# Optimization experiments

Measured on AMD Instinct MI355X. Metric: run time of the kernel, lower is better.

## Reference

```python
import jax, jax.numpy as jnp
import numpy as np

MASK_VAL = -1e30


def setup_inputs() -> dict:
    key = jax.random.key(0)
    ks = jax.random.split(key, 9)
    B, C, Q, D = 64, 2048, 128, 128
    s = 0.05  # small param init scale (xavier-like)
    return {
        "vfeats": jax.random.normal(ks[0], (B, C, D), jnp.float32),
        "qfeats": jax.random.normal(ks[1], (B, Q, D), jnp.float32),
        "vmask": jnp.ones((B, C), jnp.float32),
        "qmask": jnp.ones((B, Q), jnp.float32),
        "w4C": jax.random.normal(ks[2], (D, 1), jnp.float32) * s,
        "w4Q": jax.random.normal(ks[3], (D, 1), jnp.float32) * s,
        "w4mlu": jax.random.normal(ks[4], (1, 1, D), jnp.float32) * s,
        "cqa_W": jax.random.normal(ks[5], (D, 4 * D), jnp.float32) * s,  # Conv1D k=1 == Linear(4D->D)
        "cqa_b": jnp.zeros((D,), jnp.float32),
        "wp": jax.random.normal(ks[6], (D, 1), jnp.float32) * s,
        "cc_W": jax.random.normal(ks[7], (D, 2 * D), jnp.float32) * s,  # Conv1D k=1 == Linear(2D->D)
        "cc_b": jnp.zeros((D,), jnp.float32),
    }


def reference(vfeats, qfeats, vmask, qmask, w4C, w4Q, w4mlu, cqa_W, cqa_b, wp, cc_W, cc_b):
    # --- CQAttention ---
    # trilinear score: [B, C, Q]  (dropout is identity at inference)
    score = (vfeats @ w4C) \
        + jnp.swapaxes(qfeats @ w4Q, 1, 2) \
        + jnp.einsum('bcd,bqd->bcq', vfeats * w4mlu, qfeats)
    score_ = jax.nn.softmax(score + (1.0 - qmask[:, None, :]) * MASK_VAL, axis=2)   # [B,C,Q]
    score_t = jax.nn.softmax(score + (1.0 - vmask[:, :, None]) * MASK_VAL, axis=1)  # [B,C,Q]
    c2q = score_ @ qfeats                                                           # [B,C,D]
    # q2c = (score_ @ score_t^T) @ context; reassociate to avoid the [B,C,C] matrix
    q2c = score_ @ jnp.einsum('bcq,bcd->bqd', score_t, vfeats)                      # [B,C,D]
    cat = jnp.concatenate([vfeats, c2q, vfeats * c2q, vfeats * q2c], axis=2)        # [B,C,4D]
    feats = cat @ cqa_W.T + cqa_b                                                   # [B,C,D]
    # --- CQConcatenate (weighted pool of query) ---
    alpha = jax.nn.softmax((qfeats @ wp) + (1.0 - qmask[:, :, None]) * MASK_VAL, axis=1)  # [B,Q,1]
    pooled = jnp.einsum('bqd,bq->bd', qfeats, alpha[..., 0])                        # [B,D]
    pooled = jnp.broadcast_to(pooled[:, None, :], feats.shape)                      # [B,C,D]
    out = jnp.concatenate([feats, pooled], axis=2) @ cc_W.T + cc_b                  # [B,C,D]
    return jax.nn.relu(out)
```

## Files before the change

### kernel.cpp

```cpp
#include <hip/hip_runtime.h>
#include <stdint.h>

#define DI __device__ __forceinline__

typedef __attribute__((ext_vector_type(8))) short short8;
typedef __attribute__((ext_vector_type(4))) short short4v;
typedef __attribute__((ext_vector_type(4))) float float4v;
typedef __attribute__((ext_vector_type(2))) float float2v;
typedef __attribute__((ext_vector_type(4))) unsigned int uint4v;
typedef __attribute__((ext_vector_type(2))) unsigned int uint2v;
typedef __attribute__((ext_vector_type(2))) __bf16 bf162;

#define MFMA16(a, b, c) __builtin_amdgcn_mfma_f32_16x16x32_bf16((a), (b), (c), 0, 0, 0)

DI float b2f(short s) {
    uint32_t u = ((uint32_t)(uint16_t)s) << 16;
    float f;
    __builtin_memcpy(&f, &u, 4);
    return f;
}
DI unsigned int cvtpk(float a, float b) {
    bf162 h = __builtin_convertvector((float2v){a, b}, bf162);
    return __builtin_bit_cast(unsigned int, h);
}
DI float u2f(unsigned int u) { return __builtin_bit_cast(float, u); }


__global__ __launch_bounds__(256) void k_packfuse(const float* __restrict__ vf, const float* __restrict__ qf,
                                                  const float* __restrict__ w4C, const float* __restrict__ w4Q,
                                                  const float* __restrict__ w4mlu, const float* __restrict__ vmask,
                                                  const float* __restrict__ qmask, short* __restrict__ vfA,
                                                  short* __restrict__ vfT, short* __restrict__ qfBW,
                                                  short* __restrict__ qTf, float* __restrict__ cvp,
                                                  float* __restrict__ qvp, const float* __restrict__ cqaW,
                                                  short* __restrict__ cqaWp, const float* __restrict__ ccW,
                                                  short* __restrict__ ccWp, const float* __restrict__ wp,
                                                  const float* __restrict__ ccb, float* __restrict__ pc) {
    __shared__ float St[32 * 133];
    __shared__ float Rd[128], Af[128], Pp[2][128], Pl[128];
    int bx = blockIdx.x, by = blockIdx.y;
    int t = threadIdx.x;
    if (bx == 69) {
        if (by < 32) {
            int idx = by * 256 + t;
            int lane = idx & 63, ks = (idx >> 6) & 3, part = (idx >> 8) & 3, nt = idx >> 10;
            const float* p = cqaW + (size_t)(nt * 16 + (lane & 15)) * 512 + part * 128 + ks * 32 + (lane >> 4) * 8;
            float4v a = *(const float4v*)p, b = *(const float4v*)(p + 4);
            uint4v ou;
            ou[0] = cvtpk(a[0], a[1]);
            ou[1] = cvtpk(a[2], a[3]);
            ou[2] = cvtpk(b[0], b[1]);
            ou[3] = cvtpk(b[2], b[3]);
            *(short8*)(cqaWp + (size_t)idx * 8) = __builtin_bit_cast(short8, ou);
        } else if (by < 40) {
            int idx = (by - 32) * 256 + t;
            int lane = idx & 63, ks = (idx >> 6) & 3, ot = idx >> 8;
            const float* p = ccW + (size_t)(ot * 16 + (lane & 15)) * 256 + ks * 32 + (lane >> 4) * 8;
            float4v a = *(const float4v*)p, b = *(const float4v*)(p + 4);
            uint4v ou;
            ou[0] = cvtpk(a[0], a[1]);
            ou[1] = cvtpk(a[2], a[3]);
            ou[2] = cvtpk(b[0], b[1]);
            ou[3] = cvtpk(b[2], b[3]);
            *(short8*)(ccWp + (size_t)idx * 8) = __builtin_bit_cast(short8, ou);
        }
        return;
    }
    if (bx == 68) {
        int b = by;
        int q = t >> 1, hf = t & 1;
        const float* qrow = qf + ((size_t)(b * 128 + q) << 7) + hf * 64;
        float s = 0.f;
#pragma unroll 4
        for (int d = 0; d < 64; d += 4) {
            float4v xv = *(const float4v*)(qrow + d);
            float4v wg = *(const float4v*)(wp + hf * 64 + d);
            s += xv[0] * wg[0] + xv[1] * wg[1] + xv[2] * wg[2] + xv[3] * wg[3];
        }
        s += __shfl_xor(s, 1, 64);
        s += (1.f - qmask[b * 128 + q]) * (-1e30f);
        if (hf == 0) Rd[q] = s;
        __syncthreads();
        for (int off = 64; off >= 1; off >>= 1) {
            if (t < off) Rd[t] = fmaxf(Rd[t], Rd[t + off]);
            __syncthreads();
        }
        float m = Rd[0];
        __syncthreads();
        float e = __expf(s - m);
        if (hf == 0) Rd[q] = e;
        __syncthreads();
        for (int off = 64; off >= 1; off >>= 1) {
            if (t < off) Rd[t] += Rd[t + off];
            __syncthreads();
        }
        if (hf == 0) Af[q] = e * __builtin_amdgcn_rcpf(Rd[0]);
        __syncthreads();
        {
            int d = t & 127, qh = t >> 7;
            float pacc = 0.f;
            for (int qq = qh * 64; qq < qh * 64 + 64; ++qq) pacc += qf[((size_t)(b * 128 + qq) << 7) + d] * Af[qq];
            Pp[qh][d] = pacc;
        }
        __syncthreads();
        if (t < 128) Pl[t] = Pp[0][t] + Pp[1][t];
        __syncthreads();
        {
            int o = t & 127, dh = t >> 7;
            float acc = 0.f;
            for (int d = dh * 64; d < dh * 64 + 64; ++d) acc += Pl[d] * ccW[o * 256 + 128 + d];
            Pp[dh][o] = acc;
        }
        __syncthreads();
        if (t < 128) pc[b * 128 + t] = ccb[t] + Pp[0][t] + Pp[1][t];
        return;
    }
    const float* src;
    const float* wm;
    const float* wv;
    const float* mask;
    short* dstA;
    short* dstT;
    float* dotout;
    int kc, nkc, b = by;
    if (bx < 64) {
        src = vf; wm = nullptr; wv = w4C; mask = vmask;
        dstA = vfA; dstT = vfT; dotout = cvp; kc = bx; nkc = 64;
    } else {
        src = qf; wm = w4mlu; wv = w4Q; mask = qmask;
        dstA = qfBW; dstT = qTf; dotout = qvp; kc = bx - 64; nkc = 4;
    }
    int rl = t >> 3, sub = t & 7, dseg = sub * 16;
    int grow = (b * nkc + kc) * 32 + rl;
    const float* p = src + ((size_t)grow << 7) + dseg;
    float4v v[4];
#pragma unroll
    for (int g = 0; g < 4; ++g) v[g] = *(const float4v*)(p + g * 4);
    float s = 0.f;
#pragma unroll
    for (int g = 0; g < 4; ++g) {
        float4v wg = *(const float4v*)(wv + dseg + g * 4);
#pragma unroll
        for (int j = 0; j < 4; ++j) s += v[g][j] * wg[j];
    }
#pragma unroll
    for (int off = 1; off < 8; off <<= 1) s += __shfl_xor(s, off, 64);
    if (sub == 0) dotout[grow] = s + (1.f - mask[grow]) * (-1e30f);
#pragma unroll
    for (int g = 0; g < 4; ++g)
#pragma unroll
        for (int j = 0; j < 4; ++j) St[rl * 133 + dseg + g * 4 + j] = v[g][j];
#pragma unroll
    for (int h = 0; h < 2; ++h) {
        int c16 = sub * 2 + h;
        int ks = c16 >> 2, quad = c16 & 3;
        float4v m0 = wm ? *(const float4v*)(wm + c16 * 8) : (float4v){1.f, 1.f, 1.f, 1.f};
        float4v m1 = wm ? *(const float4v*)(wm + c16 * 8 + 4) : (float4v){1.f, 1.f, 1.f, 1.f};
        uint4v ou;
        ou[0] = cvtpk(v[h * 2][0] * m0[0], v[h * 2][1] * m0[1]);
        ou[1] = cvtpk(v[h * 2][2] * m0[2], v[h * 2][3] * m0[3]);
        ou[2] = cvtpk(v[h * 2 + 1][0] * m1[0], v[h * 2 + 1][1] * m1[1]);
        ou[3] = cvtpk(v[h * 2 + 1][2] * m1[2], v[h * 2 + 1][3] * m1[3]);
        int tile = b * (nkc * 2) + kc * 2 + (rl >> 4);
        *(short8*)(dstA + ((size_t)(tile * 4 + ks) << 9) + (quad * 16 + (rl & 15)) * 8) =
            __builtin_bit_cast(short8, ou);
    }
    __syncthreads();
#pragma unroll
    for (int i = 0; i < 2; ++i) {
        int dt = (t >> 6) + i * 4;
        int lane = t & 63, ln = lane & 15, quad = lane >> 4;
        int d = dt * 16 + ln;
        uint4v ou;
#pragma unroll
        for (int wd = 0; wd < 4; ++wd)
            ou[wd] = cvtpk(St[(quad * 8 + 2 * wd) * 133 + d], St[(quad * 8 + 2 * wd + 1) * 133 + d]);
        *(short8*)(dstT + (((size_t)(b * 8 + dt) * nkc + kc) << 9) + lane * 8) = __builtin_bit_cast(short8, ou);
    }
}

__global__ __launch_bounds__(256) void k_Tacc(const short* __restrict__ vfA, const short* __restrict__ vfT,
                                              const short* __restrict__ qfBW, const float* __restrict__ cvp,
                                              float* __restrict__ Pg, float* __restrict__ Csg) {
    __shared__ short Al[16 * 136];
    __shared__ float Red[4][16][130];
    __shared__ float csred[4][16];
    int tid = threadIdx.x, w = tid >> 6, lane = tid & 63, ln = lane & 15, quad = lane >> 4;
    int id = blockIdx.x;
    int xcd = id & 7, k = id >> 3;
    int g = xcd * 16 + (k & 15);
    int qt = k >> 4;
    int b = g & 63, s = g >> 6;
    short8 bq[4];
#pragma unroll
    for (int ks = 0; ks < 4; ++ks) bq[ks] = *(const short8*)(qfBW + (((size_t)(b * 8 + qt) * 4 + ks) << 9) + lane * 8);
    float4v acc[8];
#pragma unroll
    for (int dt = 0; dt < 8; ++dt) acc[dt] = (float4v){0.f, 0.f, 0.f, 0.f};
    float colacc = 0.f;
    for (int it = 0; it < 8; ++it) {
        int cbase = s * 1024 + it * 128 + w * 32;
        int ct = b * 128 + (cbase >> 4);
        short8 bb[8];
#pragma unroll
        for (int dt = 0; dt < 8; ++dt)
            bb[dt] = *(const short8*)(vfT + (((size_t)(b * 8 + dt) * 64 + s * 32 + it * 4 + w) << 9) + lane * 8);
        __builtin_amdgcn_sched_barrier(0);
        float4v ds[2];
        ds[0] = (float4v){0.f, 0.f, 0.f, 0.f};
        ds[1] = (float4v){0.f, 0.f, 0.f, 0.f};
#pragma unroll
        for (int ks = 0; ks < 4; ++ks) {
#pragma unroll
            for (int mt = 0; mt < 2; ++mt) {
                short8 a = *(const short8*)(vfA + (((size_t)(ct + mt) * 4 + ks) << 9) + lane * 8);
                ds[mt] = MFMA16(a, bq[ks], ds[mt]);
            }
        }
#pragma unroll
        for (int mt = 0; mt < 2; ++mt) {
            float4v cv = *(const float4v*)(cvp + b * 2048 + cbase + mt * 16 + quad * 4);
            float e0 = __expf(ds[mt][0] + cv[0]);
            float e1 = __expf(ds[mt][1] + cv[1]);
            float e2 = __expf(ds[mt][2] + cv[2]);
            float e3 = __expf(ds[mt][3] + cv[3]);
            colacc += e0 + e1 + e2 + e3;
            uint2v eu;
            eu[0] = cvtpk(e0, e1);
            eu[1] = cvtpk(e2, e3);
            *(short4v*)(Al + ln * 136 + w * 32 + mt * 16 + quad * 4) = __builtin_bit_cast(short4v, eu);
        }
        short8 a = *(const short8*)(Al + ln * 136 + w * 32 + quad * 8);
#pragma unroll
        for (int dt = 0; dt < 8; ++dt) acc[dt] = MFMA16(a, bb[dt], acc[dt]);
    }
#pragma unroll
    for (int dt = 0; dt < 8; ++dt)
#pragma unroll
        for (int r = 0; r < 4; ++r) Red[w][quad * 4 + r][dt * 16 + ln] = acc[dt][r];
    float p = colacc;
    p += __shfl_xor(p, 16, 64);
    p += __shfl_xor(p, 32, 64);
    if (lane < 16) csred[w][lane] = p;
    __syncthreads();
    if (tid < 16)
        Csg[((size_t)(s * 64 + b)) * 128 + qt * 16 + tid] =
            csred[0][tid] + csred[1][tid] + csred[2][tid] + csred[3][tid];
    {
        int q = tid >> 4, db = (tid & 15) * 8;
        float4v s0, s1;
#pragma unroll
        for (int j = 0; j < 4; ++j) {
            s0[j] = Red[0][q][db + j] + Red[1][q][db + j] + Red[2][q][db + j] + Red[3][q][db + j];
            s1[j] = Red[0][q][db + 4 + j] + Red[1][q][db + 4 + j] + Red[2][q][db + 4 + j] + Red[3][q][db + 4 + j];
        }
        size_t pb = (((size_t)(s * 64 + b)) * 8 + qt) * 2048 + q * 128 + db;
        *(float4v*)(Pg + pb) = s0;
        *(float4v*)(Pg + pb + 4) = s1;
    }
}

__global__ __launch_bounds__(256) void k_Tcomb(const float* __restrict__ Pg, const float* __restrict__ Csg,
                                               short* __restrict__ Ttf) {
    int idx = blockIdx.x * 256 + threadIdx.x;
    int lane = idx & 63, dt = (idx >> 8) & 7, b = idx >> 11;
    int d = dt * 16 + (lane & 15), q0 = ((idx >> 6) & 3) * 32 + (lane >> 4) * 8;
    float pv[8];
#pragma unroll
    for (int j = 0; j < 8; ++j) {
        int q = q0 + j;
        size_t o0 = ((size_t)(b * 8) + (q >> 4)) * 2048 + (q & 15) * 128 + d;
        size_t o1 = ((size_t)((64 + b) * 8) + (q >> 4)) * 2048 + (q & 15) * 128 + d;
        float cs = Csg[b * 128 + q] + Csg[(64 + b) * 128 + q];
        pv[j] = (Pg[o0] + Pg[o1]) * __builtin_amdgcn_rcpf(cs);
    }
    uint4v ou;
#pragma unroll
    for (int wd = 0; wd < 4; ++wd) ou[wd] = cvtpk(pv[2 * wd], pv[2 * wd + 1]);
    *(short8*)(Ttf + (size_t)idx * 8) = __builtin_bit_cast(short8, ou);
}

__global__ __launch_bounds__(256, 4) void k_out(const short* __restrict__ vfA, const short* __restrict__ qfBW,
                                                const short* __restrict__ qTf, const short* __restrict__ Ttf,
                                                const float* __restrict__ qvp, const short* __restrict__ cqaWp,
                                                const float* __restrict__ cqab, const short* __restrict__ ccWp,
                                                const float* __restrict__ pc, float* __restrict__ out) {
    __shared__ __align__(16) short Sl[64 * 128];
    __shared__ __align__(16) short Xl[64 * 128];
    int tid = threadIdx.x, w = tid >> 6, lane = tid & 63, ln = lane & 15, quad = lane >> 4;
    int jl = ln & 7, hi8 = ln >> 3;
    const float4v z4 = {0.f, 0.f, 0.f, 0.f};
    int id = blockIdx.x;
    int xcd = id & 7, k = id >> 3;
    int b = xcd * 8 + (k & 7);
    int cx = k >> 3;
    int c0 = cx * 64 + w * 16;
    int tt = b * 128 + (c0 >> 4);
    int wbase = w * 2048;
    {
        float4v sc[8];
#pragma unroll
        for (int qt = 0; qt < 8; ++qt) sc[qt] = z4;
#pragma unroll
        for (int ks = 0; ks < 4; ++ks) {
            short8 bqf[8];
#pragma unroll
            for (int qt = 0; qt < 8; ++qt)
                bqf[qt] = *(const short8*)(qfBW + (((size_t)(b * 8 + qt) * 4 + ks) << 9) + lane * 8);
            short8 av = *(const short8*)(vfA + (((size_t)tt * 4 + ks) << 9) + lane * 8);
#pragma unroll
            for (int qt = 0; qt < 8; ++qt) sc[qt] = MFMA16(av, bqf[qt], sc[qt]);
        }
        float qvl[8];
#pragma unroll
        for (int qt = 0; qt < 8; ++qt) qvl[qt] = qvp[b * 128 + qt * 16 + ln];
        short8 p2[8];
#pragma unroll
        for (int dt = 0; dt < 8; ++dt)
            p2[dt] = *(const short8*)(qTf + (((size_t)(b * 8 + dt) * 4 + 0) << 9) + lane * 8);
        __builtin_amdgcn_sched_barrier(0);
#pragma unroll
        for (int r = 0; r < 4; ++r) {
            float x[8], m = -3.4e38f;
#pragma unroll
            for (int qt = 0; qt < 8; ++qt) {
                x[qt] = sc[qt][r] + qvl[qt];
                m = fmaxf(m, x[qt]);
            }
#pragma unroll
            for (int off = 1; off < 16; off <<= 1) m = fmaxf(m, __shfl_xor(m, off, 64));
            float e[8], sm = 0.f;
#pragma unroll
            for (int qt = 0; qt < 8; ++qt) {
                e[qt] = __expf(x[qt] - m);
                sm += e[qt];
            }
#pragma unroll
            for (int off = 1; off < 16; off <<= 1) sm += __shfl_xor(sm, off, 64);
            float inv = __builtin_amdgcn_rcpf(sm);
            int rb = (quad * 4 + r) * 8 + jl;
#pragma unroll
            for (int qp = 0; qp < 4; ++qp) {
                unsigned int u = cvtpk(e[2 * qp] * inv, e[2 * qp + 1] * inv);
                Sl[wbase + qp * 512 + hi8 * 128 + rb] = (short)u;
                Sl[wbase + qp * 512 + (2 + hi8) * 128 + rb] = (short)(u >> 16);
            }
        }
        short8 sa[4];
#pragma unroll
        for (int ks = 0; ks < 4; ++ks) sa[ks] = *(const short8*)(Sl + wbase + ks * 512 + lane * 8);
        float4v a2q[8];
#pragma unroll
        for (int dt = 0; dt < 8; ++dt) a2q[dt] = MFMA16(sa[0], p2[dt], z4);
#pragma unroll
        for (int ks = 1; ks < 4; ++ks) {
            short8 bf[8];
#pragma unroll
            for (int dt = 0; dt < 8; ++dt)
                bf[dt] = *(const short8*)(qTf + (((size_t)(b * 8 + dt) * 4 + ks) << 9) + lane * 8);
#pragma unroll
            for (int dt = 0; dt < 8; ++dt) a2q[dt] = MFMA16(sa[ks], bf[dt], a2q[dt]);
        }
        short8 p3[8];
#pragma unroll
        for (int dt = 0; dt < 8; ++dt)
            p3[dt] = *(const short8*)(Ttf + (((size_t)(b * 8 + dt) * 4 + 0) << 9) + lane * 8);
        __builtin_amdgcn_sched_barrier(0);
#pragma unroll
        for (int r = 0; r < 4; ++r) {
            int rb = (quad * 4 + r) * 8 + jl;
#pragma unroll
            for (int dp = 0; dp < 4; ++dp) {
                unsigned int u = cvtpk(a2q[2 * dp][r], a2q[2 * dp + 1][r]);
                Xl[wbase + dp * 512 + hi8 * 128 + rb] = (short)u;
                Xl[wbase + dp * 512 + (2 + hi8) * 128 + rb] = (short)(u >> 16);
            }
        }
        float4v aq2[8];
#pragma unroll
        for (int dt = 0; dt < 8; ++dt) aq2[dt] = MFMA16(sa[0], p3[dt], z4);
#pragma unroll
        for (int ks = 1; ks < 4; ++ks) {
            short8 bf[8];
#pragma unroll
            for (int dt = 0; dt < 8; ++dt)
                bf[dt] = *(const short8*)(Ttf + (((size_t)(b * 8 + dt) * 4 + ks) << 9) + lane * 8);
#pragma unroll
            for (int dt = 0; dt < 8; ++dt) aq2[dt] = MFMA16(sa[ks], bf[dt], aq2[dt]);
        }
#pragma unroll
        for (int r = 0; r < 4; ++r) {
            int rb = (quad * 4 + r) * 8 + jl;
#pragma unroll
            for (int dp = 0; dp < 4; ++dp) {
                unsigned int u = cvtpk(aq2[2 * dp][r], aq2[2 * dp + 1][r]);
                Sl[wbase + dp * 512 + hi8 * 128 + rb] = (short)u;
                Sl[wbase + dp * 512 + (2 + hi8) * 128 + rb] = (short)(u >> 16);
            }
        }
    }
    __syncthreads();
    float4v accF[4][2];
#pragma unroll
    for (int ct = 0; ct < 4; ++ct)
#pragma unroll
        for (int nt2 = 0; nt2 < 2; ++nt2) accF[ct][nt2] = z4;
#pragma unroll
    for (int ks = 0; ks < 4; ++ks) {
        short8 avk[4];
#pragma unroll
        for (int ct = 0; ct < 4; ++ct)
            avk[ct] = *(const short8*)(vfA + (((size_t)(b * 128 + cx * 4 + ct) * 4 + ks) << 9) + lane * 8);
#pragma unroll
        for (int part = 0; part < 4; ++part) {
            short8 bwp[2];
#pragma unroll
            for (int nt2 = 0; nt2 < 2; ++nt2)
                bwp[nt2] =
                    *(const short8*)(cqaWp + (((size_t)((w * 2 + nt2) * 4 + part) * 4 + ks) << 9) + lane * 8);
            short8 a[4];
#pragma unroll
            for (int ct = 0; ct < 4; ++ct) {
                int fo = ct * 2048 + ks * 512 + lane * 8;
                if (part == 0) {
                    a[ct] = avk[ct];
                } else if (part == 1) {
                    a[ct] = *(const short8*)(Xl + fo);
                } else {
                    short8 mfr = (part == 2) ? *(const short8*)(Xl + fo) : *(const short8*)(Sl + fo);
                    uint4v ua = __builtin_bit_cast(uint4v, avk[ct]);
                    uint4v um = __builtin_bit_cast(uint4v, mfr);
                    uint4v uo;
#pragma unroll
                    for (int wd = 0; wd < 4; ++wd) {
                        float a0 = u2f(ua[wd] << 16), a1 = u2f(ua[wd] & 0xffff0000u);
                        float m0 = u2f(um[wd] << 16), m1 = u2f(um[wd] & 0xffff0000u);
                        uo[wd] = cvtpk(a0 * m0, a1 * m1);
                    }
                    a[ct] = __builtin_bit_cast(short8, uo);
                }
            }
#pragma unroll
            for (int nt2 = 0; nt2 < 2; ++nt2)
#pragma unroll
                for (int ct = 0; ct < 4; ++ct) accF[ct][nt2] = MFMA16(a[ct], bwp[nt2], accF[ct][nt2]);
        }
    }
    __syncthreads();
    {
        float b0 = cqab[(w * 2) * 16 + ln], b1 = cqab[(w * 2 + 1) * 16 + ln];
#pragma unroll
        for (int ct = 0; ct < 4; ++ct)
#pragma unroll
            for (int r = 0; r < 4; ++r) {
                unsigned int u = cvtpk(accF[ct][0][r] + b0, accF[ct][1][r] + b1);
                int rb = ct * 2048 + w * 512 + (quad * 4 + r) * 8 + jl;
                Sl[rb + hi8 * 128] = (short)u;
                Sl[rb + (2 + hi8) * 128] = (short)(u >> 16);
            }
    }
    __syncthreads();
    float4v accO[4][2];
#pragma unroll
    for (int ct = 0; ct < 4; ++ct)
#pragma unroll
        for (int ot2 = 0; ot2 < 2; ++ot2) accO[ct][ot2] = z4;
#pragma unroll
    for (int ks = 0; ks < 4; ++ks) {
        short8 bwo[2];
#pragma unroll
        for (int ot2 = 0; ot2 < 2; ++ot2)
            bwo[ot2] = *(const short8*)(ccWp + (((size_t)((w * 2 + ot2) * 4 + ks)) << 9) + lane * 8);
        short8 a[4];
#pragma unroll
        for (int ct = 0; ct < 4; ++ct) a[ct] = *(const short8*)(Sl + ct * 2048 + ks * 512 + lane * 8);
#pragma unroll
        for (int ot2 = 0; ot2 < 2; ++ot2)
#pragma unroll
            for (int ct = 0; ct < 4; ++ct) accO[ct][ot2] = MFMA16(a[ct], bwo[ot2], accO[ct][ot2]);
    }
#pragma unroll
    for (int ct = 0; ct < 4; ++ct)
#pragma unroll
        for (int ot2 = 0; ot2 < 2; ++ot2) {
            int o = (w * 2 + ot2) * 16 + ln;
            float pco = pc[b * 128 + o];
#pragma unroll
            for (int r = 0; r < 4; ++r) {
                int c = cx * 64 + ct * 16 + quad * 4 + r;
                out[((size_t)(b * 2048 + c) << 7) + o] = fmaxf(accO[ct][ot2][r] + pco, 0.f);
            }
        }
}

extern "C" void kernel_launch(void* const* d_in, const int* in_sizes, int n_in, void* d_out, int out_size, void* d_ws,
                              size_t ws_size, hipStream_t stream) {
    const float* vf = (const float*)d_in[0];
    const float* qf = (const float*)d_in[1];
    const float* vmask = (const float*)d_in[2];
    const float* qmask = (const float*)d_in[3];
    const float* w4C = (const float*)d_in[4];
    const float* w4Q = (const float*)d_in[5];
    const float* w4mlu = (const float*)d_in[6];
    const float* cqaW = (const float*)d_in[7];
    const float* cqab = (const float*)d_in[8];
    const float* wp = (const float*)d_in[9];
    const float* ccW = (const float*)d_in[10];
    const float* ccb = (const float*)d_in[11];
    float* out = (float*)d_out;
    char* ws = (char*)d_ws;

    size_t o = 0;
    short* vfA = (short*)(ws + o); o += 64ull * 2048 * 128 * 2;
    short* vfT = (short*)(ws + o); o += 64ull * 2048 * 128 * 2;
    short* qfBW = (short*)(ws + o); o += 64ull * 128 * 128 * 2;
    short* qTf = (short*)(ws + o); o += 64ull * 128 * 128 * 2;
    short* Ttf = (short*)(ws + o); o += 64ull * 128 * 128 * 2;
    short* cqaWp = (short*)(ws + o); o += 128ull * 512 * 2;
    short* ccWp = (short*)(ws + o); o += 128ull * 128 * 2;
    float* Pg = (float*)(ws + o); o += 2ull * 64 * 128 * 128 * 4;
    float* Csg = (float*)(ws + o); o += 2ull * 64 * 128 * 4;
    float* cvp = (float*)(ws + o); o += 64ull * 2048 * 4;
    float* qvp = (float*)(ws + o); o += 64ull * 128 * 4;
    float* pc = (float*)(ws + o); o += 64ull * 128 * 4;

    k_packfuse<<<dim3(70, 64), 256, 0, stream>>>(vf, qf, w4C, w4Q, w4mlu, vmask, qmask, vfA, vfT, qfBW, qTf, cvp,
                                                 qvp, cqaW, cqaWp, ccW, ccWp, wp, ccb, pc);
    k_Tacc<<<1024, 256, 0, stream>>>(vfA, vfT, qfBW, cvp, Pg, Csg);
    k_Tcomb<<<512, 256, 0, stream>>>(Pg, Csg, Ttf);
    k_out<<<2048, 256, 0, stream>>>(vfA, qfBW, qTf, Ttf, qvp, cqaWp, cqab, ccWp, pc, out);
}
```

Baseline: 270.1 us.

## Process two query tiles per block in k_Tacc to reuse context loads

Each k_Tacc block now handles two 16-query tiles instead of one, so the vfA and vfT fragments it loads are shared by both tiles' MFMAs. The grid halves to 512 blocks, and a launch bound of 3 blocks per SM is added. The per-block partial reduction now loops over the two tiles with extra barriers. The aim is to halve global and L2 traffic for the context operand, at the cost of more registers per thread and fewer blocks for latency hiding.

```diff
diff --git a/kernel.cpp b/kernel.cpp
--- a/kernel.cpp
+++ b/kernel.cpp
@@ -179,84 +179,105 @@
     }
 }
 
-__global__ __launch_bounds__(256) void k_Tacc(const short* __restrict__ vfA, const short* __restrict__ vfT,
-                                              const short* __restrict__ qfBW, const float* __restrict__ cvp,
-                                              float* __restrict__ Pg, float* __restrict__ Csg) {
-    __shared__ short Al[16 * 136];
+__global__ __launch_bounds__(256, 3) void k_Tacc(const short* __restrict__ vfA, const short* __restrict__ vfT,
+                                                 const short* __restrict__ qfBW, const float* __restrict__ cvp,
+                                                 float* __restrict__ Pg, float* __restrict__ Csg) {
+    __shared__ __align__(16) short Al[2][16 * 136];
     __shared__ float Red[4][16][130];
-    __shared__ float csred[4][16];
+    __shared__ float csred[2][4][16];
     int tid = threadIdx.x, w = tid >> 6, lane = tid & 63, ln = lane & 15, quad = lane >> 4;
     int id = blockIdx.x;
     int xcd = id & 7, k = id >> 3;
     int g = xcd * 16 + (k & 15);
-    int qt = k >> 4;
+    int qp = k >> 4;
     int b = g & 63, s = g >> 6;
-    short8 bq[4];
-#pragma unroll
-    for (int ks = 0; ks < 4; ++ks) bq[ks] = *(const short8*)(qfBW + (((size_t)(b * 8 + qt) * 4 + ks) << 9) + lane * 8);
-    float4v acc[8];
-#pragma unroll
-    for (int dt = 0; dt < 8; ++dt) acc[dt] = (float4v){0.f, 0.f, 0.f, 0.f};
-    float colacc = 0.f;
+    short8 bq[2][4];
+#pragma unroll
+    for (int qi = 0; qi < 2; ++qi)
+#pragma unroll
+        for (int ks = 0; ks < 4; ++ks)
+            bq[qi][ks] = *(const short8*)(qfBW + (((size_t)(b * 8 + qp * 2 + qi) * 4 + ks) << 9) + lane * 8);
+    float4v acc[2][8];
+#pragma unroll
+    for (int qi = 0; qi < 2; ++qi)
+#pragma unroll
+        for (int dt = 0; dt < 8; ++dt) acc[qi][dt] = (float4v){0.f, 0.f, 0.f, 0.f};
+    float colacc[2] = {0.f, 0.f};
     for (int it = 0; it < 8; ++it) {
         int cbase = s * 1024 + it * 128 + w * 32;
         int ct = b * 128 + (cbase >> 4);
-        short8 bb[8];
-#pragma unroll
-        for (int dt = 0; dt < 8; ++dt)
-            bb[dt] = *(const short8*)(vfT + (((size_t)(b * 8 + dt) * 64 + s * 32 + it * 4 + w) << 9) + lane * 8);
-        __builtin_amdgcn_sched_barrier(0);
-        float4v ds[2];
-        ds[0] = (float4v){0.f, 0.f, 0.f, 0.f};
-        ds[1] = (float4v){0.f, 0.f, 0.f, 0.f};
+        float4v ds[2][2];
+#pragma unroll
+        for (int qi = 0; qi < 2; ++qi) {
+            ds[qi][0] = (float4v){0.f, 0.f, 0.f, 0.f};
+            ds[qi][1] = (float4v){0.f, 0.f, 0.f, 0.f};
+        }
 #pragma unroll
         for (int ks = 0; ks < 4; ++ks) {
-#pragma unroll
-            for (int mt = 0; mt < 2; ++mt) {
-                short8 a = *(const short8*)(vfA + (((size_t)(ct + mt) * 4 + ks) << 9) + lane * 8);
-                ds[mt] = MFMA16(a, bq[ks], ds[mt]);
-            }
+            short8 va0 = *(const short8*)(vfA + (((size_t)(ct + 0) * 4 + ks) << 9) + lane * 8);
+            short8 va1 = *(const short8*)(vfA + (((size_t)(ct + 1) * 4 + ks) << 9) + lane * 8);
+            ds[0][0] = MFMA16(va0, bq[0][ks], ds[0][0]);
+            ds[0][1] = MFMA16(va1, bq[0][ks], ds[0][1]);
+            ds[1][0] = MFMA16(va0, bq[1][ks], ds[1][0]);
+            ds[1][1] = MFMA16(va1, bq[1][ks], ds[1][1]);
         }
 #pragma unroll
         for (int mt = 0; mt < 2; ++mt) {
             float4v cv = *(const float4v*)(cvp + b * 2048 + cbase + mt * 16 + quad * 4);
-            float e0 = __expf(ds[mt][0] + cv[0]);
-            float e1 = __expf(ds[mt][1] + cv[1]);
-            float e2 = __expf(ds[mt][2] + cv[2]);
-            float e3 = __expf(ds[mt][3] + cv[3]);
-            colacc += e0 + e1 + e2 + e3;
-            uint2v eu;
-            eu[0] = cvtpk(e0, e1);
-            eu[1] = cvtpk(e2, e3);
-            *(short4v*)(Al + ln * 136 + w * 32 + mt * 16 + quad * 4) = __builtin_bit_cast(short4v, eu);
-        }
-        short8 a = *(const short8*)(Al + ln * 136 + w * 32 + quad * 8);
-#pragma unroll
-        for (int dt = 0; dt < 8; ++dt) acc[dt] = MFMA16(a, bb[dt], acc[dt]);
-    }
-#pragma unroll
-    for (int dt = 0; dt < 8; ++dt)
-#pragma unroll
-        for (int r = 0; r < 4; ++r) Red[w][quad * 4 + r][dt * 16 + ln] = acc[dt][r];
-    float p = colacc;
-    p += __shfl_xor(p, 16, 64);
-    p += __shfl_xor(p, 32, 64);
-    if (lane < 16) csred[w][lane] = p;
+#pragma unroll
+            for (int qi = 0; qi < 2; ++qi) {
+                float e0 = __expf(ds[qi][mt][0] + cv[0]);
+                float e1 = __expf(ds[qi][mt][1] + cv[1]);
+                float e2 = __expf(ds[qi][mt][2] + cv[2]);
+                float e3 = __expf(ds[qi][mt][3] + cv[3]);
+                colacc[qi] += e0 + e1 + e2 + e3;
+                uint2v eu;
+                eu[0] = cvtpk(e0, e1);
+                eu[1] = cvtpk(e2, e3);
+                *(short4v*)(Al[qi] + ln * 136 + w * 32 + mt * 16 + quad * 4) = __builtin_bit_cast(short4v, eu);
+            }
+        }
+        short8 a0 = *(const short8*)(Al[0] + ln * 136 + w * 32 + quad * 8);
+        short8 a1 = *(const short8*)(Al[1] + ln * 136 + w * 32 + quad * 8);
+#pragma unroll
+        for (int dt = 0; dt < 8; ++dt) {
+            short8 bb = *(const short8*)(vfT + (((size_t)(b * 8 + dt) * 64 + s * 32 + it * 4 + w) << 9) + lane * 8);
+            acc[0][dt] = MFMA16(a0, bb, acc[0][dt]);
+            acc[1][dt] = MFMA16(a1, bb, acc[1][dt]);
+        }
+    }
+#pragma unroll
+    for (int qi = 0; qi < 2; ++qi) {
+        float p = colacc[qi];
+        p += __shfl_xor(p, 16, 64);
+        p += __shfl_xor(p, 32, 64);
+        if (lane < 16) csred[qi][w][lane] = p;
+    }
     __syncthreads();
-    if (tid < 16)
-        Csg[((size_t)(s * 64 + b)) * 128 + qt * 16 + tid] =
-            csred[0][tid] + csred[1][tid] + csred[2][tid] + csred[3][tid];
-    {
-        int q = tid >> 4, db = (tid & 15) * 8;
-        float4v s0, s1;
-#pragma unroll
-        for (int j = 0; j < 4; ++j) {
-            s0[j] = Red[0][q][db + j] + Red[1][q][db + j] + Red[2][q][db + j] + Red[3][q][db + j];
-            s1[j] = Red[0][q][db + 4 + j] + Red[1][q][db + 4 + j] + Red[2][q][db + 4 + j] + Red[3][q][db + 4 + j];
-        }
-        size_t pb = (((size_t)(s * 64 + b)) * 8 + qt) * 2048 + q * 128 + db;
-        *(float4v*)(Pg + pb) = s0;
-        *(float4v*)(Pg + pb + 4) = s1;
+    if (tid < 32) {
+        int qi = tid >> 4, q = tid & 15;
+        Csg[((size_t)(s * 64 + b)) * 128 + (qp * 2 + qi) * 16 + q] =
+            csred[qi][0][q] + csred[qi][1][q] + csred[qi][2][q] + csred[qi][3][q];
+    }
+    for (int qi = 0; qi < 2; ++qi) {
+#pragma unroll
+        for (int dt = 0; dt < 8; ++dt)
+#pragma unroll
+            for (int r = 0; r < 4; ++r) Red[w][quad * 4 + r][dt * 16 + ln] = acc[qi][dt][r];
+        __syncthreads();
+        {
+            int q = tid >> 4, db = (tid & 15) * 8;
+            float4v s0, s1;
+#pragma unroll
+            for (int j = 0; j < 4; ++j) {
+                s0[j] = Red[0][q][db + j] + Red[1][q][db + j] + Red[2][q][db + j] + Red[3][q][db + j];
+                s1[j] = Red[0][q][db + 4 + j] + Red[1][q][db + 4 + j] + Red[2][q][db + 4 + j] + Red[3][q][db + 4 + j];
+            }
+            size_t pb = (((size_t)(s * 64 + b)) * 8 + qp * 2 + qi) * 2048 + q * 128 + db;
+            *(float4v*)(Pg + pb) = s0;
+            *(float4v*)(Pg + pb + 4) = s1;
+        }
+        __syncthreads();
     }
 }
 
@@ -526,7 +547,7 @@
 
     k_packfuse<<<dim3(70, 64), 256, 0, stream>>>(vf, qf, w4C, w4Q, w4mlu, vmask, qmask, vfA, vfT, qfBW, qTf, cvp,
                                                  qvp, cqaW, cqaWp, ccW, ccWp, wp, ccb, pc);
-    k_Tacc<<<1024, 256, 0, stream>>>(vfA, vfT, qfBW, cvp, Pg, Csg);
+    k_Tacc<<<512, 256, 0, stream>>>(vfA, vfT, qfBW, cvp, Pg, Csg);
     k_Tcomb<<<512, 256, 0, stream>>>(Pg, Csg, Ttf);
     k_out<<<2048, 256, 0, stream>>>(vfA, qfBW, qTf, Ttf, qvp, cqaWp, cqab, ccWp, pc, out);
 }
```

Result: faster. 255.0 us (-5.6%).
